# Kernel tuning notes

Hardware: AMD Instinct MI355X
Metric: run time of the kernel (lower is better)

The kernel has to match this reference:

```python
import jax, jax.numpy as jnp
import numpy as np

N, E, D = 20000, 320000, 128
TD, AD, RH, Z = 16, 16, 256, 64
RIN = 2 * RH // 2 + TD + AD  # 256 + 16 + 16 = 288


def _w(k, shape):
    # torch-style [out, in] weight, scaled by 1/sqrt(fan_in)
    return jax.random.normal(k, shape, jnp.float32) / np.sqrt(shape[-1])


def setup_inputs() -> dict:
    key = jax.random.key(0)
    ks = jax.random.split(key, 32)
    inp = {
        "x": jax.random.normal(ks[0], (N, D), jnp.float32),
        "t": jax.random.normal(ks[1], (N, TD), jnp.float32),
        "a": jax.random.normal(ks[2], (N, AD), jnp.float32),
        "eps": jax.random.normal(ks[3], (N, Z), jnp.float32),
        "edge_index": jax.random.randint(ks[4], (2, E), 0, N, jnp.int64)
        if jax.config.jax_enable_x64 else jax.random.randint(ks[4], (2, E), 0, N, jnp.int32),
        "enc_w1": _w(ks[5], (256, 2 * D)), "enc_b1": jnp.zeros((256,), jnp.float32),
        "enc_w2": _w(ks[6], (256, 256)), "enc_b2": jnp.zeros((256,), jnp.float32),
        "hi_w0": _w(ks[7], (RH, 288)), "hi_b0": jnp.zeros((RH,), jnp.float32),
        "hi_w1": _w(ks[8], (RH, 288)), "hi_b1": jnp.zeros((RH,), jnp.float32),
        "gru_wih0": _w(ks[9], (3 * RH, 288)), "gru_whh0": _w(ks[10], (3 * RH, RH)),
        "gru_bih0": jnp.zeros((3 * RH,), jnp.float32), "gru_bhh0": jnp.zeros((3 * RH,), jnp.float32),
        "gru_wih1": _w(ks[11], (3 * RH, RH)), "gru_whh1": _w(ks[12], (3 * RH, RH)),
        "gru_bih1": jnp.zeros((3 * RH,), jnp.float32), "gru_bhh1": jnp.zeros((3 * RH,), jnp.float32),
        "mu_w": _w(ks[13], (Z, RH)), "mu_b": jnp.zeros((Z,), jnp.float32),
        "lv_w": _w(ks[14], (Z, RH)), "lv_b": jnp.zeros((Z,), jnp.float32),
    }
    return inp


def _gru_cell(xin, h, wih, whh, bih, bhh):
    gi = xin @ wih.T + bih          # [N, 3H]
    gh = h @ whh.T + bhh            # [N, 3H]
    i_r, i_z, i_n = jnp.split(gi, 3, axis=-1)
    h_r, h_z, h_n = jnp.split(gh, 3, axis=-1)
    r = jax.nn.sigmoid(i_r + h_r)
    zg = jax.nn.sigmoid(i_z + h_z)
    n = jnp.tanh(i_n + r * h_n)
    return (1.0 - zg) * n + zg * h


def reference(x, t, a, eps, edge_index,
              enc_w1, enc_b1, enc_w2, enc_b2,
              hi_w0, hi_b0, hi_w1, hi_b1,
              gru_wih0, gru_whh0, gru_bih0, gru_bhh0,
              gru_wih1, gru_whh1, gru_bih1, gru_bhh1,
              mu_w, mu_b, lv_w, lv_b):
    n_nodes = x.shape[0]
    src, dst = edge_index[0], edge_index[1]
    # EdgeConv: nn(cat([x_i, x_j - x_i])) with max aggregation at target i
    x_i = x[dst]                                   # [E, D]
    x_j = x[src]                                   # [E, D]
    m = jnp.concatenate([x_i, x_j - x_i], axis=-1)  # [E, 2D]
    m = jax.nn.relu(m @ enc_w1.T + enc_b1)
    m = jax.nn.relu(m @ enc_w2.T + enc_b2)          # [E, 256]
    agg = jax.ops.segment_max(m, dst, num_segments=n_nodes)
    agg = jnp.where(jnp.isneginf(agg), 0.0, agg)    # nodes w/o edges -> 0
    feat = jnp.concatenate([agg, t, a], axis=-1)    # [N, 288]
    # initial hidden per GRU layer from rnn_hi MLPs (h is None branch)
    h0 = jnp.tanh(feat @ hi_w0.T + hi_b0)           # [N, 256]
    h1 = jnp.tanh(feat @ hi_w1.T + hi_b1)
    # single GRU step, 2 layers (nodes act as batch)
    new_h0 = _gru_cell(feat, h0, gru_wih0, gru_whh0, gru_bih0, gru_bhh0)
    new_h1 = _gru_cell(new_h0, h1, gru_wih1, gru_whh1, gru_bih1, gru_bhh1)
    h = jnp.stack([new_h0, new_h1], axis=0)         # [2, N, 256]
    data = new_h1
    mu = data @ mu_w.T + mu_b                        # [N, 64]
    log_var = data @ lv_w.T + lv_b
    std = jnp.exp(0.5 * log_var)
    z = mu + eps * std
    return h, mu, log_var, z
```

## Files before the change

kernel.cpp:

```cpp
#include <hip/hip_runtime.h>
#include <math.h>

#define N_NODES 20000
#define N_EDGES 320000

typedef __attribute__((ext_vector_type(8))) short bf16x8;
typedef __attribute__((ext_vector_type(4))) float f32x4;
typedef unsigned short ushort_t;
typedef unsigned int uint_t;

__device__ __forceinline__ float bf2f(uint_t u) {
    uint_t i = u << 16; float f; __builtin_memcpy(&f, &i, 4); return f;
}
__device__ __forceinline__ ushort_t f2bf(float f) {
    uint_t i; __builtin_memcpy(&i, &f, 4);
    uint_t r = i + 0x7fffu + ((i >> 16) & 1u);
    return (ushort_t)(r >> 16);
}

__global__ void pack_all(const float* __restrict__ w1, const float* __restrict__ b1,
                         const float* __restrict__ w2,
                         const float* __restrict__ hiw0, const float* __restrict__ hiw1,
                         const float* __restrict__ wih0, const float* __restrict__ whh0,
                         const float* __restrict__ wih1, const float* __restrict__ whh1,
                         const float* __restrict__ muw, const float* __restrict__ lvw,
                         const float* __restrict__ mub, const float* __restrict__ lvb,
                         ushort_t* __restrict__ pk, float* __restrict__ bpq)
{
    const int w = blockIdx.y;
    const int i = blockIdx.x * 256 + threadIdx.x;
    if (w == 9) {
        if (i < 256)      bpq[i] = b1[i];
        else if (i < 512) bpq[i] = 0.0f;
        else if (i < 576) bpq[i] = mub[i - 512];
        else if (i < 640) bpq[i] = lvb[i - 576];
        return;
    }
    const int Ks[9]  = {128, 256, 288, 288, 288, 256, 256, 256, 256};
    const int NOs[9] = {512, 256, 256, 256, 768, 768, 768, 768, 128};
    const int DST[9] = {0, 65536, 131072, 204800, 278528, 499712, 696320, 892928, 1089536};
    const float* srcs[9] = {w1, w2, hiw0, hiw1, wih0, whh0, wih1, whh1, muw};
    const int K = Ks[w], NO = NOs[w];
    if (i >= (K * NO) >> 3) return;
    const int lane = i & 63, rest = i >> 6, NOT = NO >> 4;
    const int ot = rest % NOT, k0 = rest / NOT;
    const int row = ot * 16 + (lane & 15);
    const int kb = k0 * 32 + (lane >> 4) * 8;
    ushort_t o[8];
    if (w == 0) {
#pragma unroll
        for (int j = 0; j < 8; ++j) {
            int k = kb + j;
            float v = (row < 256) ? (w1[row * 256 + k] - w1[row * 256 + 128 + k])
                                  : w1[(row - 256) * 256 + 128 + k];
            o[j] = f2bf(v);
        }
    } else if (w == 8) {
#pragma unroll
        for (int j = 0; j < 8; ++j) {
            float v = (row < 64) ? muw[row * 256 + kb + j] : lvw[(row - 64) * 256 + kb + j];
            o[j] = f2bf(v);
        }
    } else {
        const float* s = srcs[w];
#pragma unroll
        for (int j = 0; j < 8; ++j) o[j] = f2bf(s[(size_t)row * K + kb + j]);
    }
    ushort_t* d = pk + DST[w] + (size_t)i * 8;
    ((uint_t*)d)[0] = (uint_t)o[0] | ((uint_t)o[1] << 16);
    ((uint_t*)d)[1] = (uint_t)o[2] | ((uint_t)o[3] << 16);
    ((uint_t*)d)[2] = (uint_t)o[4] | ((uint_t)o[5] << 16);
    ((uint_t*)d)[3] = (uint_t)o[6] | ((uint_t)o[7] << 16);
}

__global__ void xcvt(const float* __restrict__ x, ushort_t* __restrict__ xbf)
{
    int base = (blockIdx.x * 256 + threadIdx.x) * 4;
    if (base >= N_NODES * 128) return;
    float4 v = *(const float4*)&x[base];
    uint2 u;
    u.x = (uint_t)f2bf(v.x) | ((uint_t)f2bf(v.y) << 16);
    u.y = (uint_t)f2bf(v.z) | ((uint_t)f2bf(v.w) << 16);
    *(uint2*)&xbf[base] = u;
}

template <int BN, int OMODE>
__global__ __launch_bounds__(256) void mgemm(
    const ushort_t* __restrict__ Abf, int lda, int M, int K,
    const ushort_t* __restrict__ Wp, int NOtot, const float* __restrict__ bias,
    float* __restrict__ Cf, ushort_t* __restrict__ Cbf, int ldc)
{
    __shared__ char smem[40960];
    const int tid = threadIdx.x;
    const int l = tid & 63, wid = tid >> 6;
    const int m0 = blockIdx.x * 64;
    const int n0 = blockIdx.y * BN;
    const int RS = (K * 2 + 127) & ~127;
    const int CHR = K >> 3;
    for (int c = tid; c < 64 * CHR; c += 256) {
        int row = c / CHR, cb = c - row * CHR;
        int gr = m0 + row; if (gr >= M) gr = M - 1;
        bf16x8 v = *(const bf16x8*)&Abf[(size_t)gr * lda + cb * 8];
        *(bf16x8*)&smem[row * RS + ((cb * 16) ^ ((row & 7) << 4))] = v;
    }
    __syncthreads();

    constexpr int NT = BN / 16;
    f32x4 acc[NT];
#pragma unroll
    for (int j = 0; j < NT; ++j) acc[j] = (f32x4){0.f, 0.f, 0.f, 0.f};
    const int rw = wid * 16 + (l & 15);
    const int hi = l >> 4;
    const int swz = (rw & 7) << 4;
    const int KB = K >> 5;
    const int otb = n0 >> 4;
    for (int k0 = 0; k0 < KB; ++k0) {
        bf16x8 a = *(const bf16x8*)&smem[rw * RS + ((k0 * 64 + hi * 16) ^ swz)];
        const ushort_t* wb = Wp + ((size_t)(k0 * NOtot + otb) * 64 + l) * 8;
#pragma unroll
        for (int j = 0; j < NT; ++j) {
            bf16x8 b = *(const bf16x8*)&wb[(size_t)j * 512];
            acc[j] = __builtin_amdgcn_mfma_f32_16x16x32_bf16(a, b, acc[j], 0, 0, 0);
        }
    }
    const int c0 = l & 15;
    const int r0 = m0 + wid * 16 + hi * 4;
    if (OMODE == 4) {
        const float* epsp = (const float*)Cbf;
#pragma unroll
        for (int j = 0; j < 4; ++j) {
            int c = j * 16 + c0;
            float bmu = bias[c], blv = bias[64 + c];
#pragma unroll
            for (int r = 0; r < 4; ++r) {
                int gr = r0 + r;
                if (gr >= M) continue;
                float mu = acc[j][r] + bmu;
                float lv = acc[j + 4][r] + blv;
                float e  = epsp[(size_t)gr * 64 + c];
                Cf[(size_t)gr * 64 + c] = mu;
                Cf[(size_t)M * 64 + (size_t)gr * 64 + c] = lv;
                Cf[(size_t)2 * M * 64 + (size_t)gr * 64 + c] = mu + e * expf(0.5f * lv);
            }
        }
        return;
    }
#pragma unroll
    for (int j = 0; j < NT; ++j) {
        float bj = bias[n0 + j * 16 + c0];
#pragma unroll
        for (int r = 0; r < 4; ++r) {
            int gr = r0 + r;
            if (gr >= M) continue;
            float v = acc[j][r] + bj;
            if (OMODE == 2) v = tanhf(v);
            size_t o = (size_t)gr * ldc + n0 + j * 16 + c0;
            if (OMODE == 0) Cf[o] = v;
            else if (OMODE == 1) Cbf[o] = f2bf(v);
            else { Cf[o] = v; Cbf[o] = f2bf(v); }
        }
    }
}

__global__ __launch_bounds__(256) void edge_mfma(
    const ushort_t* __restrict__ PQbf,
    const int* __restrict__ ei,
    const ushort_t* __restrict__ W2p,
    const float* __restrict__ b2,
    float* __restrict__ agg)
{
    __shared__ char h1s[16384];
    __shared__ int s_dst[32], s_src[32];
    const int tid = threadIdx.x;
    const int e0 = blockIdx.x * 32;
    if (tid < 32) {
        int d = ei[N_EDGES + e0 + tid];
        s_dst[tid] = min(max(d, 0), N_NODES - 1);
    } else if (tid < 64) {
        int s = ei[e0 + tid - 32];
        s_src[tid - 32] = min(max(s, 0), N_NODES - 1);
    }
    __syncthreads();

    const int wv = tid >> 6;
    const int ln = tid & 63;
#pragma unroll 4
    for (int eb = wv; eb < 32; eb += 4) {
        int dst = s_dst[eb], src = s_src[eb];
        uint2 pu = *(const uint2*)&PQbf[(size_t)dst * 512 + ln * 4];
        uint2 qu = *(const uint2*)&PQbf[(size_t)src * 512 + 256 + ln * 4];
        float v0 = fmaxf(bf2f(pu.x & 0xffffu) + bf2f(qu.x & 0xffffu), 0.f);
        float v1 = fmaxf(bf2f(pu.x >> 16)     + bf2f(qu.x >> 16),     0.f);
        float v2 = fmaxf(bf2f(pu.y & 0xffffu) + bf2f(qu.y & 0xffffu), 0.f);
        float v3 = fmaxf(bf2f(pu.y >> 16)     + bf2f(qu.y >> 16),     0.f);
        uint2 hv;
        hv.x = (uint_t)f2bf(v0) | ((uint_t)f2bf(v1) << 16);
        hv.y = (uint_t)f2bf(v2) | ((uint_t)f2bf(v3) << 16);
        *(uint2*)&h1s[eb * 512 + ((ln * 8) ^ ((eb & 7) << 4))] = hv;
    }
    __syncthreads();

    const int l = tid & 63, wid = tid >> 6;
    const int rw = (wid & 1) * 16 + (l & 15);
    const int hi = l >> 4;
    const int swz = (rw & 7) << 4;
    const int otb = (wid >> 1) * 8;
    f32x4 acc[8];
#pragma unroll
    for (int j = 0; j < 8; ++j) acc[j] = (f32x4){0.f, 0.f, 0.f, 0.f};
    for (int k0 = 0; k0 < 8; ++k0) {
        bf16x8 a = *(const bf16x8*)&h1s[rw * 512 + ((k0 * 64 + hi * 16) ^ swz)];
        const ushort_t* wb = W2p + ((size_t)(k0 * 16 + otb) * 64 + l) * 8;
#pragma unroll
        for (int j = 0; j < 8; ++j) {
            bf16x8 b = *(const bf16x8*)&wb[(size_t)j * 512];
            acc[j] = __builtin_amdgcn_mfma_f32_16x16x32_bf16(a, b, acc[j], 0, 0, 0);
        }
    }
    const int c0 = l & 15;
    const int edg = (wid & 1) * 16 + hi * 4;
#pragma unroll
    for (int j = 0; j < 8; ++j) {
        int col = (otb + j) * 16 + c0;
        float bj = b2[col];
#pragma unroll
        for (int r = 0; r < 4; ++r) {
            float v = acc[j][r] + bj;
            if (v > 0.f) {
                int node = s_dst[edg + r];
                int* addr = (int*)&agg[(size_t)node * 256 + col];
                int iv = __float_as_int(v);
                if (iv > *addr) atomicMax(addr, iv);
            }
        }
    }
}

__global__ void build_feat(const float* __restrict__ agg, const float* __restrict__ t,
                           const float* __restrict__ a, ushort_t* __restrict__ featbf)
{
    int idx = blockIdx.x * 256 + threadIdx.x;
    if (idx >= N_NODES * 288) return;
    int n = idx / 288, c = idx - n * 288;
    float v;
    if (c < 256)      v = agg[(size_t)n * 256 + c];
    else if (c < 272) v = t[n * 16 + (c - 256)];
    else              v = a[n * 16 + (c - 272)];
    featbf[idx] = f2bf(v);
}

__global__ __launch_bounds__(256) void gru_fused(
    const ushort_t* __restrict__ A1, int K1,
    const ushort_t* __restrict__ A2,
    const ushort_t* __restrict__ Wp1,
    const ushort_t* __restrict__ Wp2,
    const float* __restrict__ bih, const float* __restrict__ bhh,
    const float* __restrict__ hf,
    float* __restrict__ houtf,
    ushort_t* __restrict__ houtb)
{
    __shared__ char smem[40960];
    const int tid = threadIdx.x;
    const int l = tid & 63, wid = tid >> 6;
    const int m0 = blockIdx.x * 64;
    const int n0 = blockIdx.y * 64;
    const int rw = wid * 16 + (l & 15);
    const int hi = l >> 4;
    const int swz = (rw & 7) << 4;
    const int otb = n0 >> 4;

    f32x4 aR[4], aZ[4], aN[4], bR[4], bZ[4], bN[4];
#pragma unroll
    for (int j = 0; j < 4; ++j) {
        aR[j] = (f32x4){0.f,0.f,0.f,0.f}; aZ[j] = aR[j]; aN[j] = aR[j];
        bR[j] = aR[j]; bZ[j] = aR[j]; bN[j] = aR[j];
    }

    {
        const int RS = (K1 * 2 + 127) & ~127;
        const int CHR = K1 >> 3;
        for (int c = tid; c < 64 * CHR; c += 256) {
            int row = c / CHR, cb = c - row * CHR;
            int gr = m0 + row; if (gr >= N_NODES) gr = N_NODES - 1;
            bf16x8 v = *(const bf16x8*)&A1[(size_t)gr * K1 + cb * 8];
            *(bf16x8*)&smem[row * RS + ((cb * 16) ^ ((row & 7) << 4))] = v;
        }
        __syncthreads();
        const int KB = K1 >> 5;
        for (int k0 = 0; k0 < KB; ++k0) {
            bf16x8 a = *(const bf16x8*)&smem[rw * RS + ((k0 * 64 + hi * 16) ^ swz)];
            const ushort_t* wb = Wp1 + ((size_t)(k0 * 48) * 64 + l) * 8;
#pragma unroll
            for (int j = 0; j < 4; ++j) {
                bf16x8 b0 = *(const bf16x8*)&wb[(size_t)(otb + j) * 512];
                aR[j] = __builtin_amdgcn_mfma_f32_16x16x32_bf16(a, b0, aR[j], 0, 0, 0);
                bf16x8 b1 = *(const bf16x8*)&wb[(size_t)(16 + otb + j) * 512];
                aZ[j] = __builtin_amdgcn_mfma_f32_16x16x32_bf16(a, b1, aZ[j], 0, 0, 0);
                bf16x8 b2 = *(const bf16x8*)&wb[(size_t)(32 + otb + j) * 512];
                aN[j] = __builtin_amdgcn_mfma_f32_16x16x32_bf16(a, b2, aN[j], 0, 0, 0);
            }
        }
    }
    __syncthreads();
    {
        for (int c = tid; c < 64 * 32; c += 256) {
            int row = c >> 5, cb = c & 31;
            int gr = m0 + row; if (gr >= N_NODES) gr = N_NODES - 1;
            bf16x8 v = *(const bf16x8*)&A2[(size_t)gr * 256 + cb * 8];
            *(bf16x8*)&smem[row * 512 + ((cb * 16) ^ ((row & 7) << 4))] = v;
        }
        __syncthreads();
        for (int k0 = 0; k0 < 8; ++k0) {
            bf16x8 a = *(const bf16x8*)&smem[rw * 512 + ((k0 * 64 + hi * 16) ^ swz)];
            const ushort_t* wb = Wp2 + ((size_t)(k0 * 48) * 64 + l) * 8;
#pragma unroll
            for (int j = 0; j < 4; ++j) {
                bf16x8 b0 = *(const bf16x8*)&wb[(size_t)(otb + j) * 512];
                bR[j] = __builtin_amdgcn_mfma_f32_16x16x32_bf16(a, b0, bR[j], 0, 0, 0);
                bf16x8 b1 = *(const bf16x8*)&wb[(size_t)(16 + otb + j) * 512];
                bZ[j] = __builtin_amdgcn_mfma_f32_16x16x32_bf16(a, b1, bZ[j], 0, 0, 0);
                bf16x8 b2 = *(const bf16x8*)&wb[(size_t)(32 + otb + j) * 512];
                bN[j] = __builtin_amdgcn_mfma_f32_16x16x32_bf16(a, b2, bN[j], 0, 0, 0);
            }
        }
    }
    const int c0 = l & 15;
    const int r0 = m0 + wid * 16 + hi * 4;
#pragma unroll
    for (int j = 0; j < 4; ++j) {
        int col = n0 + j * 16 + c0;
        float br_ = bih[col], bz_ = bih[256 + col], bn_ = bih[512 + col];
        float cr_ = bhh[col], cz_ = bhh[256 + col], cn_ = bhh[512 + col];
#pragma unroll
        for (int r = 0; r < 4; ++r) {
            int gr = r0 + r;
            if (gr >= N_NODES) continue;
            float ir = aR[j][r] + br_, iz = aZ[j][r] + bz_, in_ = aN[j][r] + bn_;
            float hr = bR[j][r] + cr_, hz = bZ[j][r] + cz_, hn = bN[j][r] + cn_;
            float h = hf[(size_t)gr * 256 + col];
            float rg = 1.f / (1.f + expf(-(ir + hr)));
            float zg = 1.f / (1.f + expf(-(iz + hz)));
            float ng = tanhf(in_ + rg * hn);
            float v = (1.f - zg) * ng + zg * h;
            houtf[(size_t)gr * 256 + col] = v;
            houtb[(size_t)gr * 256 + col] = f2bf(v);
        }
    }
}

extern "C" void kernel_launch(void* const* d_in, const int* in_sizes, int n_in,
                              void* d_out, int out_size, void* d_ws, size_t ws_size,
                              hipStream_t stream)
{
    const float* x      = (const float*)d_in[0];
    const float* t      = (const float*)d_in[1];
    const float* a      = (const float*)d_in[2];
    const float* eps    = (const float*)d_in[3];
    const int*   ei     = (const int*)d_in[4];
    const float* enc_w1 = (const float*)d_in[5];
    const float* enc_b1 = (const float*)d_in[6];
    const float* enc_w2 = (const float*)d_in[7];
    const float* enc_b2 = (const float*)d_in[8];
    const float* hi_w0  = (const float*)d_in[9];
    const float* hi_b0  = (const float*)d_in[10];
    const float* hi_w1  = (const float*)d_in[11];
    const float* hi_b1  = (const float*)d_in[12];
    const float* wih0   = (const float*)d_in[13];
    const float* whh0   = (const float*)d_in[14];
    const float* bih0   = (const float*)d_in[15];
    const float* bhh0   = (const float*)d_in[16];
    const float* wih1   = (const float*)d_in[17];
    const float* whh1   = (const float*)d_in[18];
    const float* bih1   = (const float*)d_in[19];
    const float* bhh1   = (const float*)d_in[20];
    const float* mu_w   = (const float*)d_in[21];
    const float* mu_b   = (const float*)d_in[22];
    const float* lv_w   = (const float*)d_in[23];
    const float* lv_b   = (const float*)d_in[24];

    char* W = (char*)d_ws;
    ushort_t* pk     = (ushort_t*)(W + 0);
    float*    bpq    = (float*)(W + 2244608);
    ushort_t* xbf    = (ushort_t*)(W + 2247680);
    float*    agg    = (float*)(W + 7368704);
    float*    h0f    = (float*)(W + 7368704);
    ushort_t* pqbf   = (ushort_t*)(W + 27848704);
    float*    h1f    = (float*)(W + 27848704);
    ushort_t* featbf = (ushort_t*)(W + 48328704);
    ushort_t* h0bf   = (ushort_t*)(W + 59848704);
    ushort_t* h1bf   = (ushort_t*)(W + 70088704);
    ushort_t* nh0bf  = (ushort_t*)(W + 80328704);
    ushort_t* nh1bf  = (ushort_t*)(W + 90568704);

    float* out_h0 = (float*)d_out;
    float* out_h1 = out_h0 + (size_t)N_NODES * 256;
    float* out_mu = out_h1 + (size_t)N_NODES * 256;

    dim3 blk(256);

    pack_all<<<dim3(108, 10), blk, 0, stream>>>(enc_w1, enc_b1, enc_w2, hi_w0, hi_w1,
                                                wih0, whh0, wih1, whh1, mu_w, lv_w,
                                                mu_b, lv_b, pk, bpq);
    xcvt<<<2500, blk, 0, stream>>>(x, xbf);
    hipMemsetAsync(agg, 0, (size_t)N_NODES * 256 * sizeof(float), stream);

    mgemm<128, 1><<<dim3(313, 4), blk, 0, stream>>>(xbf, 128, N_NODES, 128,
                                                    pk + 0, 32, bpq, nullptr, pqbf, 512);
    edge_mfma<<<10000, blk, 0, stream>>>(pqbf, ei, pk + 65536, enc_b2, agg);

    build_feat<<<22500, blk, 0, stream>>>(agg, t, a, featbf);

    mgemm<128, 2><<<dim3(313, 2), blk, 0, stream>>>(featbf, 288, N_NODES, 288,
                                                    pk + 131072, 16, hi_b0, h0f, h0bf, 256);
    mgemm<128, 2><<<dim3(313, 2), blk, 0, stream>>>(featbf, 288, N_NODES, 288,
                                                    pk + 204800, 16, hi_b1, h1f, h1bf, 256);
    gru_fused<<<dim3(313, 4), blk, 0, stream>>>(featbf, 288, h0bf,
                                                pk + 278528, pk + 499712,
                                                bih0, bhh0, h0f, out_h0, nh0bf);
    gru_fused<<<dim3(313, 4), blk, 0, stream>>>(nh0bf, 256, h1bf,
                                                pk + 696320, pk + 892928,
                                                bih1, bhh1, h1f, out_h1, nh1bf);
    mgemm<128, 4><<<dim3(313, 1), blk, 0, stream>>>(nh1bf, 256, N_NODES, 256,
                                                    pk + 1089536, 8, bpq + 512,
                                                    out_mu, (ushort_t*)eps, 64);
}
```

Before: 803.4 us.

## Sort edges by destination and pre-reduce max before atomics

Adds a counting sort of edges by destination node (histogram, single-block scan, scatter) so edge_mfma processes edges grouped by target. In the epilogue, consecutive rows sharing a destination are max-reduced in registers before issuing one atomicMax, which cuts atomic traffic and improves locality of agg and PQ gathers. It drops the previous read-before-atomic check and adds three small kernels, including a serial-ish one-block scan, plus atomic-based scatter.

```diff
diff --git a/kernel.cpp b/kernel.cpp
--- a/kernel.cpp
+++ b/kernel.cpp
@@ -84,6 +84,46 @@
     *(uint2*)&xbf[base] = u;
 }
 
+__global__ void hist_dst(const int* __restrict__ ei, int* __restrict__ cnt)
+{
+    int idx = blockIdx.x * 256 + threadIdx.x;
+    if (idx >= N_EDGES) return;
+    int d = ei[N_EDGES + idx];
+    d = min(max(d, 0), N_NODES - 1);
+    atomicAdd(&cnt[d], 1);
+}
+
+__global__ void scan_hist(const int* __restrict__ cnt, int* __restrict__ rcur)
+{
+    __shared__ int part[256];
+    const int tidx = threadIdx.x;
+    const int beg = tidx * 79;
+    const int end = min(beg + 79, N_NODES);
+    int s = 0;
+    for (int i = beg; i < end; ++i) s += cnt[i];
+    part[tidx] = s;
+    __syncthreads();
+    for (int off = 1; off < 256; off <<= 1) {
+        int v = (tidx >= off) ? part[tidx - off] : 0;
+        __syncthreads();
+        part[tidx] += v;
+        __syncthreads();
+    }
+    int run = part[tidx] - s;
+    for (int i = beg; i < end; ++i) { int c = cnt[i]; rcur[i] = run; run += c; }
+}
+
+__global__ void scatter_edges(const int* __restrict__ ei, int* __restrict__ rcur,
+                              int* __restrict__ ssrc, int* __restrict__ sdst)
+{
+    int idx = blockIdx.x * 256 + threadIdx.x;
+    if (idx >= N_EDGES) return;
+    int d = ei[N_EDGES + idx]; d = min(max(d, 0), N_NODES - 1);
+    int s = ei[idx];           s = min(max(s, 0), N_NODES - 1);
+    int pos = atomicAdd(&rcur[d], 1);
+    sdst[pos] = d; ssrc[pos] = s;
+}
+
 template <int BN, int OMODE>
 __global__ __launch_bounds__(256) void mgemm(
     const ushort_t* __restrict__ Abf, int lda, int M, int K,
@@ -164,7 +204,8 @@
 
 __global__ __launch_bounds__(256) void edge_mfma(
     const ushort_t* __restrict__ PQbf,
-    const int* __restrict__ ei,
+    const int* __restrict__ sdst,
+    const int* __restrict__ ssrc,
     const ushort_t* __restrict__ W2p,
     const float* __restrict__ b2,
     float* __restrict__ agg)
@@ -173,13 +214,8 @@
     __shared__ int s_dst[32], s_src[32];
     const int tid = threadIdx.x;
     const int e0 = blockIdx.x * 32;
-    if (tid < 32) {
-        int d = ei[N_EDGES + e0 + tid];
-        s_dst[tid] = min(max(d, 0), N_NODES - 1);
-    } else if (tid < 64) {
-        int s = ei[e0 + tid - 32];
-        s_src[tid - 32] = min(max(s, 0), N_NODES - 1);
-    }
+    if (tid < 32)       s_dst[tid] = sdst[e0 + tid];
+    else if (tid < 64)  s_src[tid - 32] = ssrc[e0 + tid - 32];
     __syncthreads();
 
     const int wv = tid >> 6;
@@ -223,16 +259,21 @@
     for (int j = 0; j < 8; ++j) {
         int col = (otb + j) * 16 + c0;
         float bj = b2[col];
+        int nd = s_dst[edg];
+        float mx = 0.0f;
 #pragma unroll
         for (int r = 0; r < 4; ++r) {
             float v = acc[j][r] + bj;
-            if (v > 0.f) {
-                int node = s_dst[edg + r];
-                int* addr = (int*)&agg[(size_t)node * 256 + col];
-                int iv = __float_as_int(v);
-                if (iv > *addr) atomicMax(addr, iv);
+            int d2 = s_dst[edg + r];
+            if (d2 != nd) {
+                if (mx > 0.f)
+                    atomicMax((int*)&agg[(size_t)nd * 256 + col], __float_as_int(mx));
+                nd = d2; mx = 0.0f;
             }
-        }
+            mx = fmaxf(mx, v);
+        }
+        if (mx > 0.f)
+            atomicMax((int*)&agg[(size_t)nd * 256 + col], __float_as_int(mx));
     }
 }
 
@@ -391,6 +432,10 @@
     ushort_t* h1bf   = (ushort_t*)(W + 70088704);
     ushort_t* nh0bf  = (ushort_t*)(W + 80328704);
     ushort_t* nh1bf  = (ushort_t*)(W + 90568704);
+    int*      cnt    = (int*)(W + 100808704);
+    int*      rcur   = (int*)(W + 100888704);
+    int*      sdst   = (int*)(W + 100968704);
+    int*      ssrc   = (int*)(W + 102248704);
 
     float* out_h0 = (float*)d_out;
     float* out_h1 = out_h0 + (size_t)N_NODES * 256;
@@ -404,9 +449,14 @@
     xcvt<<<2500, blk, 0, stream>>>(x, xbf);
     hipMemsetAsync(agg, 0, (size_t)N_NODES * 256 * sizeof(float), stream);
 
+    hipMemsetAsync(cnt, 0, N_NODES * sizeof(int), stream);
+    hist_dst<<<(N_EDGES + 255) / 256, blk, 0, stream>>>(ei, cnt);
+    scan_hist<<<1, blk, 0, stream>>>(cnt, rcur);
+    scatter_edges<<<(N_EDGES + 255) / 256, blk, 0, stream>>>(ei, rcur, ssrc, sdst);
+
     mgemm<128, 1><<<dim3(313, 4), blk, 0, stream>>>(xbf, 128, N_NODES, 128,
                                                     pk + 0, 32, bpq, nullptr, pqbf, 512);
-    edge_mfma<<<10000, blk, 0, stream>>>(pqbf, ei, pk + 65536, enc_b2, agg);
+    edge_mfma<<<10000, blk, 0, stream>>>(pqbf, sdst, ssrc, pk + 65536, enc_b2, agg);
 
     build_feat<<<22500, blk, 0, stream>>>(agg, t, a, featbf);
 
```

After: 742.5 us. 7.6% less time.
